# Kernel optimization log

Measured on AMD Instinct MI355X. Metric: run time of the kernel, lower is better.

## Reference

```python
import jax, jax.numpy as jnp
import numpy as np

HEADS = 16
ROPE_BASE = 10000.0


def _apply_rope(x, shift=0):
    # x: [b, h, s, d]; pairs (2i, 2i+1) form complex numbers rotated by m*theta_i
    b, h, s, d = x.shape
    half = d // 2
    theta = jnp.exp(-jnp.log(ROPE_BASE) * jnp.arange(0, d, 2, dtype=jnp.float32) / d)  # [half]
    m = jnp.arange(shift, shift + s, dtype=jnp.float32)[:, None]                        # [s,1]
    freqs = m * theta[None, :]                                                          # [s,half]
    cos = jnp.cos(freqs)[None, None]                                                    # [1,1,s,half]
    sin = jnp.sin(freqs)[None, None]
    xr = x.reshape(b, h, s, half, 2)
    xe, xo = xr[..., 0], xr[..., 1]
    oe = xe * cos - xo * sin
    oo = xe * sin + xo * cos
    return jnp.stack([oe, oo], axis=-1).reshape(b, h, s, d)


def setup_inputs() -> dict:
    key = jax.random.key(0)
    ks = jax.random.split(key, 4)
    b, s, dim = 2, 2048, 2048
    x = jax.random.normal(ks[0], (b, s, dim), dtype=jnp.float32)
    Wq = jax.random.normal(ks[1], (dim, dim), dtype=jnp.float32) * 0.02
    Wk = jax.random.normal(ks[2], (dim, dim), dtype=jnp.float32) * 0.02
    Wv = jax.random.normal(ks[3], (dim, dim), dtype=jnp.float32) * 0.02
    return {"x": x, "Wq": Wq, "Wk": Wk, "Wv": Wv}


def reference(x, Wq, Wk, Wv):
    b, s, dim = x.shape
    h = HEADS
    d = dim // h
    # QKV projections (torch Linear: y = x @ W^T), split into heads: b h s d
    q = jnp.einsum('bsm,nm->bsn', x, Wq).reshape(b, s, h, d).transpose(0, 2, 1, 3)
    k = jnp.einsum('bsm,nm->bsn', x, Wk).reshape(b, s, h, d).transpose(0, 2, 1, 3)
    v = jnp.einsum('bsm,nm->bsn', x, Wv).reshape(b, s, h, d).transpose(0, 2, 1, 3)
    # RoPE (torch version is under no_grad -> detached)
    q = jax.lax.stop_gradient(_apply_rope(q.astype(jnp.float32)))
    k = jax.lax.stop_gradient(_apply_rope(k.astype(jnp.float32)))
    # causal scaled dot-product attention, fp32 softmax
    scale = 1.0 / jnp.sqrt(jnp.float32(d))
    scores = jnp.einsum('bhqd,bhkd->bhqk', q, k).astype(jnp.float32) * scale
    causal = jnp.tril(jnp.ones((s, s), dtype=bool))
    scores = jnp.where(causal[None, None], scores, jnp.float32(-1e30))
    attn = jax.nn.softmax(scores, axis=-1)
    out = jnp.einsum('bhqk,bhkd->bhqd', attn, v.astype(jnp.float32))
    # b h s d -> b s (h d)
    return out.transpose(0, 2, 1, 3).reshape(b, s, dim)
```

## Files before the change

### kernel.cpp

```cpp
#include <hip/hip_runtime.h>
#include <hip/hip_bf16.h>
#include <stdint.h>

typedef __bf16 bf16;
typedef bf16 bf16x8 __attribute__((ext_vector_type(8)));
typedef bf16 bf16x4 __attribute__((ext_vector_type(4)));
typedef float f32x4 __attribute__((ext_vector_type(4)));

#define MFMA16(a, b, c) __builtin_amdgcn_mfma_f32_16x16x32_bf16(a, b, c, 0, 0, 0)

static __device__ __forceinline__ bf16 f2b(float f) { return (bf16)f; }
static __device__ __forceinline__ float b2f(bf16 v) { return (float)v; }

static __device__ __forceinline__ void gload16(const void* src, void* dst) {
    __builtin_amdgcn_global_load_lds(
        (const __attribute__((address_space(1))) uint32_t*)src,
        (__attribute__((address_space(3))) uint32_t*)dst, 16, 0, 0);
}

__global__ void cvt_all(const float* __restrict__ x,  const float* __restrict__ wq,
                        const float* __restrict__ wk, const float* __restrict__ wv,
                        bf16* __restrict__ xb,  bf16* __restrict__ wqb,
                        bf16* __restrict__ wkb, bf16* __restrict__ wvb) {
    int i = blockIdx.x * blockDim.x + threadIdx.x;
    const float* src; bf16* dst; int off;
    if (i < 2097152)      { src = x;  dst = xb;  off = i; }
    else if (i < 3145728) { src = wq; dst = wqb; off = i - 2097152; }
    else if (i < 4194304) { src = wk; dst = wkb; off = i - 3145728; }
    else                  { src = wv; dst = wvb; off = i - 4194304; }
    float4 v = reinterpret_cast<const float4*>(src)[off];
    bf16x4 o;
    o[0] = f2b(v.x); o[1] = f2b(v.y); o[2] = f2b(v.z); o[3] = f2b(v.w);
    reinterpret_cast<bf16x4*>(dst)[off] = o;
}

__global__ void rope_table(float2* __restrict__ tbl) {
    int t = blockIdx.x * blockDim.x + threadIdx.x;
    int i = t & 63;
    int s = t >> 6;
    float theta = expf(-9.210340371976184f * (float)(2 * i) * (1.0f / 128.0f));
    float freq = (float)s * theta;
    float sv, cv;
    sincosf(freq, &sv, &cv);
    tbl[t] = make_float2(cv, sv);
}

__global__ __launch_bounds__(256) void gemm_qkv(const bf16* __restrict__ X,
                                                const bf16* __restrict__ Wq,
                                                const bf16* __restrict__ Wk,
                                                const bf16* __restrict__ Wv,
                                                bf16* __restrict__ Qm,
                                                bf16* __restrict__ Km,
                                                bf16* __restrict__ Vt,
                                                const float2* __restrict__ tbl) {
    const int K = 2048;
    __shared__ bf16 As[2][128 * 64];
    __shared__ bf16 Bs[2][128 * 64];

    const int z = blockIdx.z;
    const bf16* W = (z == 0) ? Wq : (z == 1) ? Wk : Wv;

    const int tid  = threadIdx.x;
    const int lane = tid & 63;
    const int w    = tid >> 6;
    const int wr   = (w >> 1) * 64;
    const int wc   = (w & 1) * 64;
    const int l15  = lane & 15;
    const int l4   = lane >> 4;
    const int rbase = blockIdx.x * 128;
    const int cbase = blockIdx.y * 128;

    const int srow  = lane >> 3;
    const int sslot = lane & 7;

    f32x4 acc[4][4] = {};

    auto stage = [&](int buf, int kt) {
#pragma unroll
        for (int i = 0; i < 4; ++i) {
            int c   = w * 4 + i;
            int row = c * 8 + srow;
            int gsl = sslot ^ (row & 7);
            gload16(&X[(size_t)(rbase + row) * K + kt + gsl * 8], (char*)As[buf] + c * 1024);
            gload16(&W[(size_t)(cbase + row) * K + kt + gsl * 8], (char*)Bs[buf] + c * 1024);
        }
    };

    stage(0, 0);
    __syncthreads();
    int cur = 0;

    for (int kt = 0; kt < K; kt += 64) {
        if (kt + 64 < K) stage(cur ^ 1, kt + 64);

        bf16x8 af[2][4], bfr[2][4];
#pragma unroll
        for (int ks = 0; ks < 2; ++ks) {
#pragma unroll
            for (int mi = 0; mi < 4; ++mi) {
                int r    = wr + mi * 16 + l15;
                int phys = (ks * 4 + l4) ^ (r & 7);
                af[ks][mi] = *reinterpret_cast<const bf16x8*>(
                    (char*)As[cur] + r * 128 + phys * 16);
            }
#pragma unroll
            for (int ni = 0; ni < 4; ++ni) {
                int r    = wc + ni * 16 + l15;
                int phys = (ks * 4 + l4) ^ (r & 7);
                bfr[ks][ni] = *reinterpret_cast<const bf16x8*>(
                    (char*)Bs[cur] + r * 128 + phys * 16);
            }
        }
#pragma unroll
        for (int ks = 0; ks < 2; ++ks)
#pragma unroll
            for (int mi = 0; mi < 4; ++mi)
#pragma unroll
                for (int ni = 0; ni < 4; ++ni)
                    acc[mi][ni] = MFMA16(af[ks][mi], bfr[ks][ni], acc[mi][ni]);

        __syncthreads();
        cur ^= 1;
    }

    if (z < 2) {
        bf16* Y = (z == 0) ? Qm : Km;
        const float scale = (z == 0) ? 0.1275174396094198f : 1.0f;
        const int odd = l15 & 1;
#pragma unroll
        for (int mi = 0; mi < 4; ++mi) {
            int r0 = rbase + wr + mi * 16 + l4 * 4;
#pragma unroll
            for (int i = 0; i < 4; ++i) {
                int r = r0 + i;
                int b = r >> 11, s = r & 2047;
#pragma unroll
                for (int ni = 0; ni < 4; ++ni) {
                    int n = cbase + wc + ni * 16 + l15;
                    int h = n >> 7, d = n & 127;
                    float v = acc[mi][ni][i];
                    float p = __shfl_xor(v, 1);
                    float2 cs = tbl[(s << 6) + (d >> 1)];
                    float res = v * cs.x + (odd ? p : -p) * cs.y;
                    Y[(((size_t)b * 16 + h) * 2048 + s) * 128 + d] = f2b(res * scale);
                }
            }
        }
    } else {
#pragma unroll
        for (int mi = 0; mi < 4; ++mi) {
            int r0 = rbase + wr + mi * 16 + l4 * 4;
            int b = r0 >> 11, s = r0 & 2047;
#pragma unroll
            for (int ni = 0; ni < 4; ++ni) {
                int n = cbase + wc + ni * 16 + l15;
                int h = n >> 7, d = n & 127;
                bf16x4 o;
#pragma unroll
                for (int i = 0; i < 4; ++i) o[i] = f2b(acc[mi][ni][i]);
                *reinterpret_cast<bf16x4*>(&Vt[(((size_t)b * 16 + h) * 128 + d) * 2048 + s]) = o;
            }
        }
    }
}

__global__ __launch_bounds__(256) void flash_attn(const bf16* __restrict__ Q,
                                                  const bf16* __restrict__ Km,
                                                  const bf16* __restrict__ Vt,
                                                  float* __restrict__ out) {
    __shared__ bf16 Ksh[64 * 128];
    __shared__ bf16 Vsh[128 * 64];
    __shared__ bf16 Psh[4][16 * 64];

    const int tid  = threadIdx.x;
    const int lane = tid & 63;
    const int w    = tid >> 6;
    const int l15  = lane & 15;
    const int l4   = lane >> 4;

    const int bx  = blockIdx.x;
    const int g   = (bx >> 5) & 7;
    const int seg = bx >> 8;
    const int qt  = (seg == 0) ? 31 - g : (seg == 1) ? g : (seg == 2) ? 23 - g : 8 + g;
    const int bh  = bx & 31;
    const int b   = bh >> 4, h = bh & 15;

    const bf16* Qb = Q  + (size_t)bh * 2048 * 128;
    const bf16* Kb = Km + (size_t)bh * 2048 * 128;
    const bf16* Vb = Vt + (size_t)bh * 128 * 2048;
    const int rw = qt * 64 + w * 16;

    auto stage = [&](int kvb) {
#pragma unroll
        for (int c4 = 0; c4 < 4; ++c4) {
            int c  = w * 4 + c4;
            int kr = c * 4 + (lane >> 4);
            int ks = (lane & 15) ^ (kr & 7);
            gload16((const char*)Kb + ((size_t)(kvb + kr) * 128 + ks * 8) * 2,
                    (char*)Ksh + c * 1024);
            int vr = c * 8 + (lane >> 3);
            int vs = (lane & 7) ^ (vr & 7);
            gload16((const char*)Vb + ((size_t)vr * 2048 + kvb + vs * 8) * 2,
                    (char*)Vsh + c * 1024);
        }
    };

    bf16x8 qf[4];
#pragma unroll
    for (int ks = 0; ks < 4; ++ks)
        qf[ks] = *reinterpret_cast<const bf16x8*>(
            &Qb[(size_t)(rw + l15) * 128 + ks * 32 + l4 * 8]);

    f32x4 o[8] = {};
    float mrow[4], lrow[4];
#pragma unroll
    for (int i = 0; i < 4; ++i) { mrow[i] = -1e30f; lrow[i] = 0.0f; }

    char* pw = (char*)Psh[w];

    for (int t = 0; t <= qt; ++t) {
        const int kvb = t * 64;
        __syncthreads();
        stage(kvb);
        __syncthreads();

        const char* kb = (const char*)Ksh;
        f32x4 sacc[4] = {};
        __builtin_amdgcn_s_setprio(1);
#pragma unroll
        for (int ns = 0; ns < 4; ++ns) {
            int r = ns * 16 + l15;
#pragma unroll
            for (int ks = 0; ks < 4; ++ks) {
                int phys = (ks * 4 + l4) ^ (r & 7);
                bf16x8 kf = *reinterpret_cast<const bf16x8*>(kb + r * 256 + phys * 16);
                sacc[ns] = MFMA16(qf[ks], kf, sacc[ns]);
            }
        }
        __builtin_amdgcn_s_setprio(0);

        if (t == qt) {
#pragma unroll
            for (int ns = 0; ns < 4; ++ns) {
                int col = kvb + ns * 16 + l15;
#pragma unroll
                for (int i = 0; i < 4; ++i) {
                    int row = rw + l4 * 4 + i;
                    if (col > row) sacc[ns][i] = -1e30f;
                }
            }
        }
#pragma unroll
        for (int i = 0; i < 4; ++i) {
            float sm = fmaxf(fmaxf(sacc[0][i], sacc[1][i]), fmaxf(sacc[2][i], sacc[3][i]));
            sm = fmaxf(sm, __shfl_xor(sm, 1));
            sm = fmaxf(sm, __shfl_xor(sm, 2));
            sm = fmaxf(sm, __shfl_xor(sm, 4));
            sm = fmaxf(sm, __shfl_xor(sm, 8));
            float nm    = fmaxf(mrow[i], sm);
            float alpha = __builtin_amdgcn_exp2f(mrow[i] - nm);
            mrow[i] = nm;
            float ps = 0.0f;
            int r = l4 * 4 + i;
            int f = r & 7;
#pragma unroll
            for (int ns = 0; ns < 4; ++ns) {
                float p = __builtin_amdgcn_exp2f(sacc[ns][i] - nm);
                ps += p;
                int col  = ns * 16 + l15;
                int slot = (col >> 3) ^ f;
                *(bf16*)(pw + r * 128 + slot * 16 + (col & 7) * 2) = f2b(p);
            }
            ps += __shfl_xor(ps, 1);
            ps += __shfl_xor(ps, 2);
            ps += __shfl_xor(ps, 4);
            ps += __shfl_xor(ps, 8);
            lrow[i] = lrow[i] * alpha + ps;
#pragma unroll
            for (int ds = 0; ds < 8; ++ds) o[ds][i] *= alpha;
        }
        asm volatile("s_waitcnt lgkmcnt(0)" ::: "memory");
        __builtin_amdgcn_sched_barrier(0);
        const char* vb = (const char*)Vsh;
        __builtin_amdgcn_s_setprio(1);
#pragma unroll
        for (int k2 = 0; k2 < 2; ++k2) {
            int pr   = l15;
            int phys = (k2 * 4 + l4) ^ (pr & 7);
            bf16x8 pa = *reinterpret_cast<const bf16x8*>(pw + pr * 128 + phys * 16);
#pragma unroll
            for (int ds = 0; ds < 8; ++ds) {
                int d     = ds * 16 + l15;
                int physv = (k2 * 4 + l4) ^ (d & 7);
                bf16x8 vf = *reinterpret_cast<const bf16x8*>(vb + d * 128 + physv * 16);
                o[ds] = MFMA16(pa, vf, o[ds]);
            }
        }
        __builtin_amdgcn_s_setprio(0);
    }

#pragma unroll
    for (int i = 0; i < 4; ++i) {
        float inv = 1.0f / lrow[i];
        int row = rw + l4 * 4 + i;
#pragma unroll
        for (int ds = 0; ds < 8; ++ds)
            out[((size_t)b * 2048 + row) * 2048 + h * 128 + ds * 16 + l15] = o[ds][i] * inv;
    }
}

extern "C" void kernel_launch(void* const* d_in, const int* in_sizes, int n_in,
                              void* d_out, int out_size, void* d_ws, size_t ws_size,
                              hipStream_t stream) {
    const float* x  = (const float*)d_in[0];
    const float* Wq = (const float*)d_in[1];
    const float* Wk = (const float*)d_in[2];
    const float* Wv = (const float*)d_in[3];
    float* out = (float*)d_out;
    char* ws = (char*)d_ws;

    bf16* xb   = (bf16*)(ws + 0);
    bf16* wqb  = (bf16*)(ws + 16777216);
    bf16* wkb  = (bf16*)(ws + 25165824);
    bf16* wvb  = (bf16*)(ws + 33554432);
    bf16* Qm   = (bf16*)(ws + 41943040);
    bf16* Km   = (bf16*)(ws + 58720256);
    bf16* Vt   = (bf16*)(ws + 75497472);
    float2* tbl = (float2*)(ws + 92274688);

    cvt_all<<<20480, 256, 0, stream>>>(x, Wq, Wk, Wv, xb, wqb, wkb, wvb);
    rope_table<<<512, 256, 0, stream>>>(tbl);

    dim3 gg(32, 16, 3);
    gemm_qkv<<<gg, 256, 0, stream>>>(xb, wqb, wkb, wvb, Qm, Km, Vt, tbl);

    flash_attn<<<1024, 256, 0, stream>>>(Qm, Km, Vt, out);
}
```

Measured before the change: 242.0 us.

## Compute transposed scores and move P to registers via shuffles instead of LDS

```diff
diff --git a/kernel.cpp b/kernel.cpp
--- a/kernel.cpp
+++ b/kernel.cpp
@@ -16,6 +16,12 @@
     __builtin_amdgcn_global_load_lds(
         (const __attribute__((address_space(1))) uint32_t*)src,
         (__attribute__((address_space(3))) uint32_t*)dst, 16, 0, 0);
+}
+
+static __device__ __forceinline__ uint32_t cvtpk(float lo, float hi) {
+    uint32_t r;
+    asm volatile("v_cvt_pk_bf16_f32 %0, %1, %2" : "=v"(r) : "v"(lo), "v"(hi));
+    return r;
 }
 
 __global__ void cvt_all(const float* __restrict__ x,  const float* __restrict__ wq,
@@ -164,13 +170,12 @@
     }
 }
 
-__global__ __launch_bounds__(256) void flash_attn(const bf16* __restrict__ Q,
-                                                  const bf16* __restrict__ Km,
-                                                  const bf16* __restrict__ Vt,
-                                                  float* __restrict__ out) {
+__global__ __launch_bounds__(256, 4) void flash_attn(const bf16* __restrict__ Q,
+                                                     const bf16* __restrict__ Km,
+                                                     const bf16* __restrict__ Vt,
+                                                     float* __restrict__ out) {
     __shared__ bf16 Ksh[64 * 128];
     __shared__ bf16 Vsh[128 * 64];
-    __shared__ bf16 Psh[4][16 * 64];
 
     const int tid  = threadIdx.x;
     const int lane = tid & 63;
@@ -212,11 +217,10 @@
             &Qb[(size_t)(rw + l15) * 128 + ks * 32 + l4 * 8]);
 
     f32x4 o[8] = {};
-    float mrow[4], lrow[4];
-#pragma unroll
-    for (int i = 0; i < 4; ++i) { mrow[i] = -1e30f; lrow[i] = 0.0f; }
-
-    char* pw = (char*)Psh[w];
+    float mrow = -1e30f, lrow = 0.0f;
+
+    const int xbase = l15 + ((lane >> 4) & 1) * 32;
+    const bool hiL  = (lane >> 5) & 1;
 
     for (int t = 0; t <= qt; ++t) {
         const int kvb = t * 64;
@@ -225,87 +229,108 @@
         __syncthreads();
 
         const char* kb = (const char*)Ksh;
-        f32x4 sacc[4] = {};
+        f32x4 s4[4] = {};
         __builtin_amdgcn_s_setprio(1);
 #pragma unroll
-        for (int ns = 0; ns < 4; ++ns) {
-            int r = ns * 16 + l15;
+        for (int t4 = 0; t4 < 4; ++t4) {
+            int r = t4 * 16 + l15;
 #pragma unroll
             for (int ks = 0; ks < 4; ++ks) {
                 int phys = (ks * 4 + l4) ^ (r & 7);
                 bf16x8 kf = *reinterpret_cast<const bf16x8*>(kb + r * 256 + phys * 16);
-                sacc[ns] = MFMA16(qf[ks], kf, sacc[ns]);
+                s4[t4] = MFMA16(kf, qf[ks], s4[t4]);
             }
         }
         __builtin_amdgcn_s_setprio(0);
 
         if (t == qt) {
-#pragma unroll
-            for (int ns = 0; ns < 4; ++ns) {
-                int col = kvb + ns * 16 + l15;
-#pragma unroll
-                for (int i = 0; i < 4; ++i) {
-                    int row = rw + l4 * 4 + i;
-                    if (col > row) sacc[ns][i] = -1e30f;
-                }
-            }
-        }
-#pragma unroll
-        for (int i = 0; i < 4; ++i) {
-            float sm = fmaxf(fmaxf(sacc[0][i], sacc[1][i]), fmaxf(sacc[2][i], sacc[3][i]));
-            sm = fmaxf(sm, __shfl_xor(sm, 1));
-            sm = fmaxf(sm, __shfl_xor(sm, 2));
-            sm = fmaxf(sm, __shfl_xor(sm, 4));
-            sm = fmaxf(sm, __shfl_xor(sm, 8));
-            float nm    = fmaxf(mrow[i], sm);
-            float alpha = __builtin_amdgcn_exp2f(mrow[i] - nm);
-            mrow[i] = nm;
-            float ps = 0.0f;
-            int r = l4 * 4 + i;
-            int f = r & 7;
-#pragma unroll
-            for (int ns = 0; ns < 4; ++ns) {
-                float p = __builtin_amdgcn_exp2f(sacc[ns][i] - nm);
+            int q = rw + l15;
+#pragma unroll
+            for (int t4 = 0; t4 < 4; ++t4)
+#pragma unroll
+                for (int i = 0; i < 4; ++i)
+                    if (kvb + t4 * 16 + l4 * 4 + i > q) s4[t4][i] = -1e30f;
+        }
+
+        float sm = -1e30f;
+#pragma unroll
+        for (int t4 = 0; t4 < 4; ++t4)
+#pragma unroll
+            for (int i = 0; i < 4; ++i) sm = fmaxf(sm, s4[t4][i]);
+        sm = fmaxf(sm, __shfl_xor(sm, 16));
+        sm = fmaxf(sm, __shfl_xor(sm, 32));
+        float nm    = fmaxf(mrow, sm);
+        float alpha = __builtin_amdgcn_exp2f(mrow - nm);
+        mrow = nm;
+        float ps = 0.0f;
+#pragma unroll
+        for (int t4 = 0; t4 < 4; ++t4)
+#pragma unroll
+            for (int i = 0; i < 4; ++i) {
+                float p = __builtin_amdgcn_exp2f(s4[t4][i] - nm);
+                s4[t4][i] = p;
                 ps += p;
-                int col  = ns * 16 + l15;
-                int slot = (col >> 3) ^ f;
-                *(bf16*)(pw + r * 128 + slot * 16 + (col & 7) * 2) = f2b(p);
-            }
-            ps += __shfl_xor(ps, 1);
-            ps += __shfl_xor(ps, 2);
-            ps += __shfl_xor(ps, 4);
-            ps += __shfl_xor(ps, 8);
-            lrow[i] = lrow[i] * alpha + ps;
-#pragma unroll
-            for (int ds = 0; ds < 8; ++ds) o[ds][i] *= alpha;
-        }
-        asm volatile("s_waitcnt lgkmcnt(0)" ::: "memory");
-        __builtin_amdgcn_sched_barrier(0);
+            }
+        ps += __shfl_xor(ps, 16);
+        ps += __shfl_xor(ps, 32);
+        lrow = lrow * alpha + ps;
+
+        float ai[4];
+#pragma unroll
+        for (int i = 0; i < 4; ++i)
+            ai[i] = __shfl(alpha, (lane & 48) + l4 * 4 + i);
+#pragma unroll
+        for (int ds = 0; ds < 8; ++ds)
+#pragma unroll
+            for (int i = 0; i < 4; ++i) o[ds][i] *= ai[i];
+
+        uint32_t own[8];
+#pragma unroll
+        for (int t4 = 0; t4 < 4; ++t4) {
+            own[t4 * 2 + 0] = cvtpk(s4[t4][0], s4[t4][1]);
+            own[t4 * 2 + 1] = cvtpk(s4[t4][2], s4[t4][3]);
+        }
+        bf16x8 pa[2];
+#pragma unroll
+        for (int ks2 = 0; ks2 < 2; ++ks2) {
+            union { uint32_t u[4]; bf16x8 v; } pu;
+#pragma unroll
+            for (int s = 0; s < 4; ++s) {
+                int srcl = xbase + 16 * (s >> 1);
+                uint32_t ulo = (uint32_t)__shfl((int)own[ks2 * 4 + (s & 1)], srcl);
+                uint32_t uhi = (uint32_t)__shfl((int)own[ks2 * 4 + 2 + (s & 1)], srcl);
+                pu.u[s] = hiL ? uhi : ulo;
+            }
+            pa[ks2] = pu.v;
+        }
+
         const char* vb = (const char*)Vsh;
         __builtin_amdgcn_s_setprio(1);
 #pragma unroll
         for (int k2 = 0; k2 < 2; ++k2) {
-            int pr   = l15;
-            int phys = (k2 * 4 + l4) ^ (pr & 7);
-            bf16x8 pa = *reinterpret_cast<const bf16x8*>(pw + pr * 128 + phys * 16);
 #pragma unroll
             for (int ds = 0; ds < 8; ++ds) {
                 int d     = ds * 16 + l15;
                 int physv = (k2 * 4 + l4) ^ (d & 7);
                 bf16x8 vf = *reinterpret_cast<const bf16x8*>(vb + d * 128 + physv * 16);
-                o[ds] = MFMA16(pa, vf, o[ds]);
+                o[ds] = MFMA16(pa[k2], vf, o[ds]);
             }
         }
         __builtin_amdgcn_s_setprio(0);
     }
 
+    float inv = 1.0f / lrow;
+    float iv[4];
+#pragma unroll
+    for (int i = 0; i < 4; ++i)
+        iv[i] = __shfl(inv, (lane & 48) + l4 * 4 + i);
 #pragma unroll
     for (int i = 0; i < 4; ++i) {
-        float inv = 1.0f / lrow[i];
         int row = rw + l4 * 4 + i;
 #pragma unroll
         for (int ds = 0; ds < 8; ++ds)
-            out[((size_t)b * 2048 + row) * 2048 + h * 128 + ds * 16 + l15] = o[ds][i] * inv;
+            out[((size_t)b * 2048 + row) * 2048 + h * 128 + ds * 16 + l15] =
+                o[ds][i] * iv[i];
     }
 }
 
```

Measured after the change: 216.2 us (median of 2 runs). -10.7%, faster.
